# Kernel tuning notes

Measured on AMD Instinct MI355X. Metric: run time of the kernel, lower is better.

The kernel has to match this reference:

```python
import jax, jax.numpy as jnp
import numpy as np
from jax import lax

B, N, C_IN = 8, 16384, 32
NPOINT = 1024
RADII = (0.5, 1.0)
NSAMPLES = (16, 32)
MLPS = ((35, 32, 64), (35, 64, 128))  # first dim includes +3 for use_xyz


def setup_inputs():
    key = jax.random.key(0)
    ks = jax.random.split(key, 20)
    inp = {
        'xyz': jax.random.normal(ks[0], (B, N, 3), jnp.float32),
        'features': jax.random.normal(ks[1], (B, C_IN, N), jnp.float32),
    }
    i = 2
    for bi, spec in enumerate(MLPS):
        for li in range(len(spec) - 1):
            cin, cout = spec[li], spec[li + 1]
            inp['w%d_%d' % (bi, li)] = jax.random.normal(ks[i], (cout, cin), jnp.float32) * np.float32(1.0 / np.sqrt(cin)); i += 1
            inp['s%d_%d' % (bi, li)] = jax.random.uniform(ks[i], (cout,), jnp.float32, minval=0.5, maxval=1.5); i += 1
            inp['b%d_%d' % (bi, li)] = jax.random.normal(ks[i], (cout,), jnp.float32) * 0.1; i += 1
    return inp


def _fps(xyz, npoint):
    # iterative D-FPS, start from index 0 (matches CUDA furthest_point_sampling)
    Bb, Nn, _ = xyz.shape
    def body(carry, _):
        dists, far = carry
        centroid = jnp.take_along_axis(xyz, far[:, None, None], axis=1)  # (B,1,3)
        d = jnp.sum((xyz - centroid) ** 2, axis=-1)                       # (B,N)
        dists = jnp.minimum(dists, d)
        return (dists, jnp.argmax(dists, axis=-1).astype(jnp.int32)), far
    init = (jnp.full((Bb, Nn), 1e10, jnp.float32), jnp.zeros((Bb,), jnp.int32))
    _, idx = lax.scan(body, init, None, length=npoint)
    return idx.T  # (B, npoint)


def _ball_query(dist2, radius, nsample):
    # first-nsample-in-index-order semantics of pointnet2 ball_query;
    # empty slots padded with first hit (0 if no hit at all)
    Nn = dist2.shape[-1]
    scores = jnp.where(dist2 < radius * radius, jnp.arange(Nn, dtype=jnp.int32), Nn)
    neg, _ = lax.top_k(-scores, nsample)  # nsample smallest indices
    idx = -neg
    first = jnp.where(idx[..., :1] == Nn, 0, idx[..., :1])
    return jnp.where(idx == Nn, first, idx)


def _forward(xyz, features, params):
    fwx = jnp.concatenate([xyz.transpose(0, 2, 1), features], axis=1)   # (B,3+C,N)
    fps_idx = _fps(xyz, NPOINT)                                          # (B,P) int32
    new_xyz = jnp.take_along_axis(xyz, fps_idx[:, :, None], axis=1)      # (B,P,3)
    # pairwise squared distances via gemm (B,P,N)
    xx = jnp.sum(xyz * xyz, axis=-1)
    qq = jnp.sum(new_xyz * new_xyz, axis=-1)
    dist2 = qq[:, :, None] + xx[:, None, :] - 2.0 * jnp.einsum('bpd,bnd->bpn', new_xyz, xyz)
    centers = new_xyz.transpose(0, 2, 1)[..., None]                      # (B,3,P,1)
    outs = []
    for k in range(len(RADII)):
        idx = _ball_query(dist2, RADII[k], NSAMPLES[k])                  # (B,P,S)
        grouped = jax.vmap(lambda f, i: f[:, i])(fwx, idx)               # (B,3+C,P,S)
        x = jnp.concatenate([grouped[:, :3] - centers, grouped[:, 3:]], axis=1)
        for (w, s, b) in params[k]:
            # 1x1 Conv2d (no bias) + eval-mode BN folded into (s,b) + ReLU
            x = jax.nn.relu(jnp.einsum('oc,bcps->bops', w, x) * s[None, :, None, None] + b[None, :, None, None])
        outs.append(jnp.max(x, axis=-1))                                 # max_pool over nsample
    return new_xyz, jnp.concatenate(outs, axis=1)                        # (B,P,3), (B,192,P)


def reference(xyz, features, w0_0, s0_0, b0_0, w0_1, s0_1, b0_1, w1_0, s1_0, b1_0, w1_1, s1_1, b1_1):
    params = [[(w0_0, s0_0, b0_0), (w0_1, s0_1, b0_1)],
              [(w1_0, s1_0, b1_0), (w1_1, s1_1, b1_1)]]
    return _forward(xyz, features, params)
```

## Files before the change

kernel.cpp:

```cpp
#include <hip/hip_runtime.h>

#define B 8
#define N 16384
#define C_IN 32
#define P 1024

#define R16(OP) OP(0) OP(1) OP(2) OP(3) OP(4) OP(5) OP(6) OP(7) \
                OP(8) OP(9) OP(10) OP(11) OP(12) OP(13) OP(14) OP(15)

__global__ __launch_bounds__(1024)
void fps_kernel(const float* __restrict__ xyz, float* __restrict__ new_xyz)
{
  __shared__ float2 sxy[N];
  __shared__ float rv[2][16];
  __shared__ int   ri[2][16];

  const int b = blockIdx.x;
  const int t = threadIdx.x;
  const float* xb = xyz + (size_t)b * (N * 3);

#define FPS_DECL(i) float pz##i, dm##i = 1e10f;
  R16(FPS_DECL)
#define FPS_LOAD(i) { const int n = t + (i << 10);                             \
    float x = xb[n * 3 + 0];                                                   \
    float y = xb[n * 3 + 1];                                                   \
    pz##i   = xb[n * 3 + 2];                                                   \
    asm volatile("" : "+v"(pz##i));            \
    sxy[n] = make_float2(x, y); }
  R16(FPS_LOAD)
  __syncthreads();

  int sel = 0;
  for (int iter = 0; iter < P; ++iter) {
    const float2 cxy = sxy[sel];
    const float cx = cxy.x;
    const float cy = cxy.y;
    const float cz = xb[sel * 3 + 2];
    if (t == 0) {
      size_t o = ((size_t)b * P + iter) * 3;
      new_xyz[o + 0] = cx;
      new_xyz[o + 1] = cy;
      new_xyz[o + 2] = cz;
    }
    if (iter == P - 1) break;

    float bestv = -1.0f;
    int   bi = 0;
#define FPS_STEP(i) {                                                          \
    const float2 xy = sxy[t + (i << 10)];                                      \
    float dx = __fsub_rn(xy.x, cx);                                            \
    float dy = __fsub_rn(xy.y, cy);                                            \
    float dz = __fsub_rn(pz##i, cz);                                           \
    float d  = __fadd_rn(__fadd_rn(__fmul_rn(dx, dx), __fmul_rn(dy, dy)),      \
                         __fmul_rn(dz, dz));                                   \
    dm##i = fminf(dm##i, d);                                                   \
    bool better = dm##i > bestv;                                               \
    bestv = better ? dm##i : bestv;                                            \
    bi    = better ? i      : bi; }
    R16(FPS_STEP)
    int besti = t + (bi << 10);

#pragma unroll
    for (int off = 32; off > 0; off >>= 1) {
      float ov = __shfl_xor(bestv, off);
      int   oi = __shfl_xor(besti, off);
      bool better = (ov > bestv) || (ov == bestv && oi < besti);
      bestv = better ? ov : bestv;
      besti = better ? oi : besti;
    }
    int parity = iter & 1;
    if ((t & 63) == 0) { rv[parity][t >> 6] = bestv; ri[parity][t >> 6] = besti; }
    __syncthreads();
    float gv = rv[parity][t & 15];
    int   gi = ri[parity][t & 15];
#pragma unroll
    for (int off = 8; off > 0; off >>= 1) {
      float ov = __shfl_xor(gv, off);
      int   oi = __shfl_xor(gi, off);
      bool better = (ov > gv) || (ov == gv && oi < gi);
      gv = better ? ov : gv;
      gi = better ? oi : gi;
    }
    sel = __builtin_amdgcn_readfirstlane(gi);
  }
#undef FPS_DECL
#undef FPS_LOAD
#undef FPS_STEP
}

__global__ __launch_bounds__(256) void ballq_kernel(
    const float* __restrict__ xyz, const float* __restrict__ new_xyz,
    int* __restrict__ idx0, int* __restrict__ idx1)
{
  const int wid  = blockIdx.x * 4 + (threadIdx.x >> 6);
  const int lane = threadIdx.x & 63;
  const int b = wid >> 10;
  const int p = wid & (P - 1);
  const float* xb = xyz + (size_t)b * (N * 3);
  const size_t bp = (size_t)b * P + p;
  const float cx = new_xyz[bp * 3 + 0];
  const float cy = new_xyz[bp * 3 + 1];
  const float cz = new_xyz[bp * 3 + 2];
  const float qv = __fadd_rn(__fadd_rn(__fmul_rn(cx, cx), __fmul_rn(cy, cy)),
                             __fmul_rn(cz, cz));
  int* __restrict__ o0 = idx0 + bp * 16;
  int* __restrict__ o1 = idx1 + bp * 32;

  int c0 = 0, c1 = 0, f0 = 0, f1 = 0;
  const unsigned long long below = (1ull << lane) - 1ull;

  for (int base = 0; base < N; base += 64) {
    int n = base + lane;
    float x = xb[n * 3 + 0], y = xb[n * 3 + 1], z = xb[n * 3 + 2];
    float xxv = __fadd_rn(__fadd_rn(__fmul_rn(x, x), __fmul_rn(y, y)),
                          __fmul_rn(z, z));
    float dot = __fadd_rn(__fadd_rn(__fmul_rn(cx, x), __fmul_rn(cy, y)),
                          __fmul_rn(cz, z));
    float d2 = __fsub_rn(__fadd_rn(qv, xxv), __fmul_rn(2.0f, dot));
    unsigned long long m0 = __ballot(d2 < 0.25f);
    unsigned long long m1 = __ballot(d2 < 1.0f);
    if (c0 == 0 && m0) f0 = base + __builtin_ctzll(m0);
    if (c1 == 0 && m1) f1 = base + __builtin_ctzll(m1);
    if ((m0 >> lane) & 1ull) {
      int pos = c0 + (int)__builtin_popcountll(m0 & below);
      if (pos < 16) o0[pos] = n;
    }
    if ((m1 >> lane) & 1ull) {
      int pos = c1 + (int)__builtin_popcountll(m1 & below);
      if (pos < 32) o1[pos] = n;
    }
    c0 = min(16, c0 + (int)__builtin_popcountll(m0));
    c1 = min(32, c1 + (int)__builtin_popcountll(m1));
    if (c0 >= 16 && c1 >= 32) break;
  }
  for (int s = c0 + lane; s < 16; s += 64) o0[s] = f0;
  for (int s = c1 + lane; s < 32; s += 64) o1[s] = f1;
}

template <int S, int C1, int C2, int CH_OFF>
__global__ __launch_bounds__(256) void mlp_kernel(
    const float* __restrict__ xyz, const float* __restrict__ feats,
    const float* __restrict__ new_xyz, const int* __restrict__ idx,
    const float* __restrict__ w1, const float* __restrict__ s1,
    const float* __restrict__ b1, const float* __restrict__ w2,
    const float* __restrict__ s2, const float* __restrict__ b2,
    float* __restrict__ out)
{
  static_assert((C1 * S) % 256 == 0 && (C2 * S) % 256 == 0, "mapping");
  __shared__ float wl1[35][C1];
  __shared__ float wl2[C1][C2];
  __shared__ float sb1[2][C1];
  __shared__ float sb2[2][C2];
  __shared__ float xs[35][S];
  __shared__ float o1s[C1][S];
  __shared__ float pm[256];

  const int tid = threadIdx.x;
  for (int i = tid; i < 35 * C1; i += 256) {
    int o = i % C1, c = i / C1;
    wl1[c][o] = w1[o * 35 + c];
  }
  for (int i = tid; i < C1 * C2; i += 256) {
    int o = i % C2, c = i / C2;
    wl2[c][o] = w2[o * C1 + c];
  }
  if (tid < C1) { sb1[0][tid] = s1[tid]; sb1[1][tid] = b1[tid]; }
  if (tid < C2) { sb2[0][tid] = s2[tid]; sb2[1][tid] = b2[tid]; }

  const int b  = blockIdx.x / (P / 8);
  const int p0 = (blockIdx.x % (P / 8)) * 8;
  const float* xb = xyz + (size_t)b * (N * 3);
  const float* fb = feats + (size_t)b * (C_IN * N);
  __syncthreads();

  for (int pi = 0; pi < 8; ++pi) {
    const int p = p0 + pi;
    const size_t bp = (size_t)b * P + p;
    const int* ip = idx + bp * S;
    const float cx = new_xyz[bp * 3 + 0];
    const float cy = new_xyz[bp * 3 + 1];
    const float cz = new_xyz[bp * 3 + 2];
    for (int i = tid; i < 35 * S; i += 256) {
      int c = i / S, s = i % S;
      int n = ip[s];
      float v;
      if (c == 0)      v = xb[n * 3 + 0] - cx;
      else if (c == 1) v = xb[n * 3 + 1] - cy;
      else if (c == 2) v = xb[n * 3 + 2] - cz;
      else             v = fb[(size_t)(c - 3) * N + n];
      xs[c][s] = v;
    }
    __syncthreads();
    {
      constexpr int OPT = (C1 * S) / 256;
      const int s  = tid % S;
      const int ob = (tid / S) * OPT;
      float acc[OPT];
#pragma unroll
      for (int j = 0; j < OPT; ++j) acc[j] = 0.0f;
      for (int c = 0; c < 35; ++c) {
        float xv = xs[c][s];
#pragma unroll
        for (int j = 0; j < OPT; ++j) acc[j] = fmaf(xv, wl1[c][ob + j], acc[j]);
      }
#pragma unroll
      for (int j = 0; j < OPT; ++j) {
        float v = fmaf(acc[j], sb1[0][ob + j], sb1[1][ob + j]);
        o1s[ob + j][s] = fmaxf(v, 0.0f);
      }
    }
    __syncthreads();
    {
      constexpr int NS = (C2 * S) / 256;
      const int o2 = tid % C2;
      const int sb = (tid / C2) * NS;
      float acc[NS];
#pragma unroll
      for (int j = 0; j < NS; ++j) acc[j] = 0.0f;
      for (int c = 0; c < C1; ++c) {
        float wv = wl2[c][o2];
#pragma unroll
        for (int j = 0; j < NS; ++j) acc[j] = fmaf(wv, o1s[c][sb + j], acc[j]);
      }
      const float scale = sb2[0][o2], bias = sb2[1][o2];
      float m = 0.0f;
#pragma unroll
      for (int j = 0; j < NS; ++j) {
        float v = fmaf(acc[j], scale, bias);
        m = fmaxf(m, v);
      }
      pm[tid] = m;
      __syncthreads();
      if (tid < C2) {
        float mm = pm[tid];
#pragma unroll
        for (int g = 1; g < 256 / C2; ++g) mm = fmaxf(mm, pm[tid + g * C2]);
        out[((size_t)b * 192 + CH_OFF + tid) * P + p] = mm;
      }
    }
    __syncthreads();
  }
}

extern "C" void kernel_launch(void* const* d_in, const int* in_sizes, int n_in,
                              void* d_out, int out_size, void* d_ws, size_t ws_size,
                              hipStream_t stream) {
  const float* xyz   = (const float*)d_in[0];
  const float* feats = (const float*)d_in[1];
  const float* w0_0 = (const float*)d_in[2];
  const float* s0_0 = (const float*)d_in[3];
  const float* b0_0 = (const float*)d_in[4];
  const float* w0_1 = (const float*)d_in[5];
  const float* s0_1 = (const float*)d_in[6];
  const float* b0_1 = (const float*)d_in[7];
  const float* w1_0 = (const float*)d_in[8];
  const float* s1_0 = (const float*)d_in[9];
  const float* b1_0 = (const float*)d_in[10];
  const float* w1_1 = (const float*)d_in[11];
  const float* s1_1 = (const float*)d_in[12];
  const float* b1_1 = (const float*)d_in[13];

  float* out      = (float*)d_out;
  float* new_xyz  = out;
  float* feat_out = out + (size_t)B * P * 3;

  char* w = (char*)d_ws;
  int* idx0 = (int*)w; w += (size_t)B * P * 16 * sizeof(int);
  int* idx1 = (int*)w; w += (size_t)B * P * 32 * sizeof(int);

  fps_kernel<<<dim3(B), dim3(1024), 0, stream>>>(xyz, new_xyz);
  ballq_kernel<<<dim3(B * P / 4), dim3(256), 0, stream>>>(xyz, new_xyz, idx0, idx1);
  mlp_kernel<16, 32, 64, 0><<<dim3(B * P / 8), dim3(256), 0, stream>>>(
      xyz, feats, new_xyz, idx0, w0_0, s0_0, b0_0, w0_1, s0_1, b0_1, feat_out);
  mlp_kernel<32, 64, 128, 64><<<dim3(B * P / 8), dim3(256), 0, stream>>>(
      xyz, feats, new_xyz, idx1, w1_0, s1_0, b1_0, w1_1, s1_1, b1_1, feat_out);
}
```

Before: 2.634 ms.

## Use DPP reductions in FPS and carry z through the argmax

The per-iteration argmax in the furthest-point-sampling loop now uses DPP lane permutes (quad_perm, mirrors and row broadcasts) instead of shfl_xor butterflies. The z coordinate of the winner travels with the (value, index) pair, so the next centroid no longer needs a dependent global load. Selected centroids are kept in registers by the thread whose index matches the iteration and written out once at the end, rather than by thread 0 every iteration. Distance loads are also split into two batches of eight LDS reads to improve overlap. The aim is to shorten the serial critical path of each of the 1024 iterations, at the cost of relying on GFX9-specific DPP row_bcast semantics.

After: 2.864 ms. 1.09x slower.

```diff
diff --git a/kernel.cpp b/kernel.cpp
--- a/kernel.cpp
+++ b/kernel.cpp
@@ -7,13 +7,27 @@
 
 #define R16(OP) OP(0) OP(1) OP(2) OP(3) OP(4) OP(5) OP(6) OP(7) \
                 OP(8) OP(9) OP(10) OP(11) OP(12) OP(13) OP(14) OP(15)
+#define R8A(OP) OP(0) OP(1) OP(2) OP(3) OP(4) OP(5) OP(6) OP(7)
+#define R8B(OP) OP(8) OP(9) OP(10) OP(11) OP(12) OP(13) OP(14) OP(15)
+
+template <int CTRL>
+__device__ __forceinline__ void dpp_combine(float& v, int& idx, float& z) {
+  float ov = __int_as_float(__builtin_amdgcn_update_dpp(
+      __float_as_int(v), __float_as_int(v), CTRL, 0xF, 0xF, false));
+  int oi = __builtin_amdgcn_update_dpp(idx, idx, CTRL, 0xF, 0xF, false);
+  float oz = __int_as_float(__builtin_amdgcn_update_dpp(
+      __float_as_int(z), __float_as_int(z), CTRL, 0xF, 0xF, false));
+  bool better = (ov > v) || (ov == v && oi < idx);
+  v   = better ? ov : v;
+  idx = better ? oi : idx;
+  z   = better ? oz : z;
+}
 
 __global__ __launch_bounds__(1024)
 void fps_kernel(const float* __restrict__ xyz, float* __restrict__ new_xyz)
 {
   __shared__ float2 sxy[N];
-  __shared__ float rv[2][16];
-  __shared__ int   ri[2][16];
+  __shared__ float4 rq[2][16];
 
   const int b = blockIdx.x;
   const int t = threadIdx.x;
@@ -25,67 +39,79 @@
     float x = xb[n * 3 + 0];                                                   \
     float y = xb[n * 3 + 1];                                                   \
     pz##i   = xb[n * 3 + 2];                                                   \
-    asm volatile("" : "+v"(pz##i));            \
+    asm volatile("" : "+v"(pz##i));     \
     sxy[n] = make_float2(x, y); }
   R16(FPS_LOAD)
+
+  float cz = xb[2];
   __syncthreads();
-
-  int sel = 0;
+  float2 c0 = sxy[0];
+  float cx = c0.x, cy = c0.y;
+  float mx = 0.f, my = 0.f, mz = 0.f;
+
   for (int iter = 0; iter < P; ++iter) {
-    const float2 cxy = sxy[sel];
-    const float cx = cxy.x;
-    const float cy = cxy.y;
-    const float cz = xb[sel * 3 + 2];
-    if (t == 0) {
-      size_t o = ((size_t)b * P + iter) * 3;
-      new_xyz[o + 0] = cx;
-      new_xyz[o + 1] = cy;
-      new_xyz[o + 2] = cz;
-    }
+    bool keep = (t == iter);
+    mx = keep ? cx : mx;
+    my = keep ? cy : my;
+    mz = keep ? cz : mz;
     if (iter == P - 1) break;
 
     float bestv = -1.0f;
     int   bi = 0;
-#define FPS_STEP(i) {                                                          \
-    const float2 xy = sxy[t + (i << 10)];                                      \
-    float dx = __fsub_rn(xy.x, cx);                                            \
-    float dy = __fsub_rn(xy.y, cy);                                            \
+    float bz = pz0;
+#define FPS_PRE(i) float2 q##i = sxy[t + (i << 10)];
+#define FPS_CALC(i) {                                                          \
+    float dx = __fsub_rn(q##i.x, cx);                                          \
+    float dy = __fsub_rn(q##i.y, cy);                                          \
     float dz = __fsub_rn(pz##i, cz);                                           \
     float d  = __fadd_rn(__fadd_rn(__fmul_rn(dx, dx), __fmul_rn(dy, dy)),      \
                          __fmul_rn(dz, dz));                                   \
     dm##i = fminf(dm##i, d);                                                   \
     bool better = dm##i > bestv;                                               \
     bestv = better ? dm##i : bestv;                                            \
-    bi    = better ? i      : bi; }
-    R16(FPS_STEP)
+    bi    = better ? i      : bi;                                              \
+    bz    = better ? pz##i  : bz; }
+    { R8A(FPS_PRE) R8A(FPS_CALC) }
+    { R8B(FPS_PRE) R8B(FPS_CALC) }
     int besti = t + (bi << 10);
 
-#pragma unroll
-    for (int off = 32; off > 0; off >>= 1) {
-      float ov = __shfl_xor(bestv, off);
-      int   oi = __shfl_xor(besti, off);
-      bool better = (ov > bestv) || (ov == bestv && oi < besti);
-      bestv = better ? ov : bestv;
-      besti = better ? oi : besti;
-    }
-    int parity = iter & 1;
-    if ((t & 63) == 0) { rv[parity][t >> 6] = bestv; ri[parity][t >> 6] = besti; }
+    dpp_combine<0xB1>(bestv, besti, bz);
+    dpp_combine<0x4E>(bestv, besti, bz);
+    dpp_combine<0x141>(bestv, besti, bz);
+    dpp_combine<0x140>(bestv, besti, bz);
+    dpp_combine<0x142>(bestv, besti, bz);
+    dpp_combine<0x143>(bestv, besti, bz);
+
+    const int par = iter & 1;
+    if ((t & 63) == 63)
+      rq[par][t >> 6] = make_float4(bestv, __int_as_float(besti), bz, 0.f);
     __syncthreads();
-    float gv = rv[parity][t & 15];
-    int   gi = ri[parity][t & 15];
-#pragma unroll
-    for (int off = 8; off > 0; off >>= 1) {
-      float ov = __shfl_xor(gv, off);
-      int   oi = __shfl_xor(gi, off);
-      bool better = (ov > gv) || (ov == gv && oi < gi);
-      gv = better ? ov : gv;
-      gi = better ? oi : gi;
-    }
-    sel = __builtin_amdgcn_readfirstlane(gi);
+
+    float4 st = rq[par][t & 15];
+    float gv = st.x;
+    int   gi = __float_as_int(st.y);
+    float gz = st.z;
+    dpp_combine<0xB1>(gv, gi, gz);
+    dpp_combine<0x4E>(gv, gi, gz);
+    dpp_combine<0x141>(gv, gi, gz);
+    dpp_combine<0x140>(gv, gi, gz);
+    int sel = __builtin_amdgcn_readfirstlane(gi);
+    cz = gz;
+    float2 nxy = sxy[sel];
+    cx = nxy.x;
+    cy = nxy.y;
+  }
+
+  {
+    size_t o = ((size_t)b * P + t) * 3;
+    new_xyz[o + 0] = mx;
+    new_xyz[o + 1] = my;
+    new_xyz[o + 2] = mz;
   }
 #undef FPS_DECL
 #undef FPS_LOAD
-#undef FPS_STEP
+#undef FPS_PRE
+#undef FPS_CALC
 }
 
 __global__ __launch_bounds__(256) void ballq_kernel(
```
